# Kernel optimization log

Hardware: AMD Instinct MI355X
Metric: run time of the kernel (lower is better)

The kernel has to match this reference:

```python
import jax, jax.numpy as jnp
import numpy as np

NEG = -jnp.finfo(jnp.float32).max


def setup_inputs() -> dict:
    key = jax.random.key(0)
    ks = jax.random.split(key, 5)
    B, N, C = 8, 1024, 768
    x = jax.random.normal(ks[0], (B, N, C), dtype=jnp.float32)
    qkv_w = jax.random.normal(ks[1], (3 * C, C), dtype=jnp.float32) * (C ** -0.5)
    qkv_b = jax.random.normal(ks[2], (3 * C,), dtype=jnp.float32) * 0.02
    proj_w = jax.random.normal(ks[3], (C, C), dtype=jnp.float32) * (C ** -0.5)
    proj_b = jax.random.normal(ks[4], (C,), dtype=jnp.float32) * 0.02
    return {"x": x, "qkv_w": qkv_w, "qkv_b": qkv_b, "proj_w": proj_w, "proj_b": proj_b, "k": 64}


def reference(x, qkv_w, qkv_b, proj_w, proj_b, k):
    B, N, C = x.shape
    H = 12
    d = C // H
    scale = d ** -0.5
    # qkv projection: [B,N,3C] -> [3,B,H,N,d]
    qkv = (x @ qkv_w.T + qkv_b).reshape(B, N, 3, H, d).transpose(2, 0, 3, 1, 4)
    q, kk, v = qkv[0], qkv[1], qkv[2]
    attn = jnp.einsum("bhqd,bhkd->bhqk", q, kk) * scale  # [B,H,N,N]
    if k > 0:
        top, _ = jax.lax.top_k(attn, k)
        vk = top[..., -1:]  # k-th largest per query row
        attn = jnp.where(attn < vk, NEG, attn)
    attn = jax.nn.softmax(attn, axis=-1)
    out = jnp.einsum("bhqk,bhkd->bhqd", attn, v)  # [B,H,N,d]
    out = out.transpose(0, 2, 1, 3).reshape(B, N, C)
    return out @ proj_w.T + proj_b
```

## Files before the change

### kernel.cpp

```cpp
#include <hip/hip_runtime.h>

constexpr int Bn = 8, Nn = 1024, Cn = 768, Hn = 12, Dn = 64;

typedef _Float16 f16x4 __attribute__((ext_vector_type(4)));
typedef _Float16 f16x8 __attribute__((ext_vector_type(8)));
typedef float    f32x4v __attribute__((ext_vector_type(4)));

__device__ __forceinline__ unsigned toOrd(float f) {
  unsigned u = __float_as_uint(f);
  return (u & 0x80000000u) ? ~u : (u | 0x80000000u);
}
__device__ __forceinline__ float invOrd(unsigned v) {
  unsigned b = (v & 0x80000000u) ? (v & 0x7FFFFFFFu) : ~v;
  return __uint_as_float(b);
}
__device__ __forceinline__ int lane_excl_cnt(unsigned long long m) {
  return __builtin_amdgcn_mbcnt_hi((unsigned)(m >> 32),
         __builtin_amdgcn_mbcnt_lo((unsigned)m, 0));
}

__device__ __forceinline__ float wave_sum_f32(float x) {
  int xi = __float_as_int(x);
  x += __int_as_float(__builtin_amdgcn_update_dpp(0, xi, 0x111, 0xF, 0xF, false)); xi = __float_as_int(x);
  x += __int_as_float(__builtin_amdgcn_update_dpp(0, xi, 0x112, 0xF, 0xF, false)); xi = __float_as_int(x);
  x += __int_as_float(__builtin_amdgcn_update_dpp(0, xi, 0x114, 0xF, 0xF, false)); xi = __float_as_int(x);
  x += __int_as_float(__builtin_amdgcn_update_dpp(0, xi, 0x118, 0xF, 0xF, false)); xi = __float_as_int(x);
  x += __int_as_float(__builtin_amdgcn_update_dpp(0, xi, 0x142, 0xA, 0xF, false)); xi = __float_as_int(x);
  x += __int_as_float(__builtin_amdgcn_update_dpp(0, xi, 0x143, 0xC, 0xF, false));
  return __int_as_float(__builtin_amdgcn_readlane(__float_as_int(x), 63));
}
__device__ __forceinline__ unsigned wave_max_u32(unsigned x) {
  int xi = (int)x;
  x = max(x, (unsigned)__builtin_amdgcn_update_dpp(xi, xi, 0x111, 0xF, 0xF, false)); xi = (int)x;
  x = max(x, (unsigned)__builtin_amdgcn_update_dpp(xi, xi, 0x112, 0xF, 0xF, false)); xi = (int)x;
  x = max(x, (unsigned)__builtin_amdgcn_update_dpp(xi, xi, 0x114, 0xF, 0xF, false)); xi = (int)x;
  x = max(x, (unsigned)__builtin_amdgcn_update_dpp(xi, xi, 0x118, 0xF, 0xF, false)); xi = (int)x;
  x = max(x, (unsigned)__builtin_amdgcn_update_dpp(xi, xi, 0x142, 0xA, 0xF, false)); xi = (int)x;
  x = max(x, (unsigned)__builtin_amdgcn_update_dpp(xi, xi, 0x143, 0xC, 0xF, false));
  return (unsigned)__builtin_amdgcn_readlane((int)x, 63);
}
__device__ __forceinline__ unsigned wave_min_u32(unsigned x) {
  int xi = (int)x;
  x = min(x, (unsigned)__builtin_amdgcn_update_dpp(xi, xi, 0x111, 0xF, 0xF, false)); xi = (int)x;
  x = min(x, (unsigned)__builtin_amdgcn_update_dpp(xi, xi, 0x112, 0xF, 0xF, false)); xi = (int)x;
  x = min(x, (unsigned)__builtin_amdgcn_update_dpp(xi, xi, 0x114, 0xF, 0xF, false)); xi = (int)x;
  x = min(x, (unsigned)__builtin_amdgcn_update_dpp(xi, xi, 0x118, 0xF, 0xF, false)); xi = (int)x;
  x = min(x, (unsigned)__builtin_amdgcn_update_dpp(xi, xi, 0x142, 0xA, 0xF, false)); xi = (int)x;
  x = min(x, (unsigned)__builtin_amdgcn_update_dpp(xi, xi, 0x143, 0xC, 0xF, false));
  return (unsigned)__builtin_amdgcn_readlane((int)x, 63);
}

__global__ __launch_bounds__(256) void qkv_gemm_mfma(
    const float* __restrict__ X, const float* __restrict__ W,
    const float* __restrict__ bias,
    _Float16* __restrict__ qhp, _Float16* __restrict__ qlp,
    _Float16* __restrict__ khp, _Float16* __restrict__ klp,
    float* __restrict__ vb)
{
  constexpr int LDH = 40;
  __shared__ _Float16 AhH[128*LDH];
  __shared__ _Float16 AhL[128*LDH];
  __shared__ _Float16 BhH[64*LDH];
  __shared__ _Float16 BhL[64*LDH];
  int t = threadIdx.x;
  int wv = t >> 6, lane = t & 63;
  int quad = lane >> 4, l16 = lane & 15;
  int mt = blockIdx.x & 63, nt = blockIdx.x >> 6;
  int m0 = mt*128, n0 = nt*64;
  const float* Ap = X + (size_t)m0*768;
  const float* Bp = W + (size_t)n0*768;
  f32x4v acc1[2][4] = {};
  f32x4v acc2[2][4] = {};
  for (int k0 = 0; k0 < 768; k0 += 32) {
    float4 av[4]; float4 bv[2];
#pragma unroll
    for (int i = 0; i < 4; ++i) {
      int q = t + i*256;
      av[i] = *(const float4*)(Ap + (size_t)(q>>3)*768 + k0 + (q&7)*4);
    }
#pragma unroll
    for (int i = 0; i < 2; ++i) {
      int q = t + i*256;
      bv[i] = *(const float4*)(Bp + (size_t)(q>>3)*768 + k0 + (q&7)*4);
    }
    __syncthreads();
#pragma unroll
    for (int i = 0; i < 4; ++i) {
      int q = t + i*256;
      f16x4 h, l;
      h[0]=(_Float16)av[i].x; h[1]=(_Float16)av[i].y;
      h[2]=(_Float16)av[i].z; h[3]=(_Float16)av[i].w;
      l[0]=(_Float16)((av[i].x-(float)h[0])*2048.0f);
      l[1]=(_Float16)((av[i].y-(float)h[1])*2048.0f);
      l[2]=(_Float16)((av[i].z-(float)h[2])*2048.0f);
      l[3]=(_Float16)((av[i].w-(float)h[3])*2048.0f);
      *(f16x4*)(&AhH[(q>>3)*LDH + (q&7)*4]) = h;
      *(f16x4*)(&AhL[(q>>3)*LDH + (q&7)*4]) = l;
    }
#pragma unroll
    for (int i = 0; i < 2; ++i) {
      int q = t + i*256;
      f16x4 h, l;
      h[0]=(_Float16)bv[i].x; h[1]=(_Float16)bv[i].y;
      h[2]=(_Float16)bv[i].z; h[3]=(_Float16)bv[i].w;
      l[0]=(_Float16)((bv[i].x-(float)h[0])*2048.0f);
      l[1]=(_Float16)((bv[i].y-(float)h[1])*2048.0f);
      l[2]=(_Float16)((bv[i].z-(float)h[2])*2048.0f);
      l[3]=(_Float16)((bv[i].w-(float)h[3])*2048.0f);
      *(f16x4*)(&BhH[(q>>3)*LDH + (q&7)*4]) = h;
      *(f16x4*)(&BhL[(q>>3)*LDH + (q&7)*4]) = l;
    }
    __syncthreads();
    f16x8 bfh[4], bfl[4];
#pragma unroll
    for (int ni = 0; ni < 4; ++ni) {
      bfh[ni] = *(f16x8*)(&BhH[(ni*16+l16)*LDH + quad*8]);
      bfl[ni] = *(f16x8*)(&BhL[(ni*16+l16)*LDH + quad*8]);
    }
#pragma unroll
    for (int mi = 0; mi < 2; ++mi) {
      f16x8 afh = *(f16x8*)(&AhH[(wv*32+mi*16+l16)*LDH + quad*8]);
      f16x8 afl = *(f16x8*)(&AhL[(wv*32+mi*16+l16)*LDH + quad*8]);
#pragma unroll
      for (int ni = 0; ni < 4; ++ni) {
        acc1[mi][ni] = __builtin_amdgcn_mfma_f32_16x16x32_f16(afh, bfh[ni], acc1[mi][ni], 0, 0, 0);
        acc2[mi][ni] = __builtin_amdgcn_mfma_f32_16x16x32_f16(afh, bfl[ni], acc2[mi][ni], 0, 0, 0);
        acc2[mi][ni] = __builtin_amdgcn_mfma_f32_16x16x32_f16(afl, bfh[ni], acc2[mi][ni], 0, 0, 0);
      }
    }
  }
  int which = n0 / Cn;
  int rem0 = n0 - which*Cn;
  int h0 = rem0 >> 6;
  float sc = which == 0 ? 0.125f : 1.0f;
#pragma unroll
  for (int ni = 0; ni < 4; ++ni) {
    float bsv = bias[n0 + ni*16 + l16];
    int dd = (ni*16 + l16) & 63;
#pragma unroll
    for (int mi = 0; mi < 2; ++mi)
#pragma unroll
      for (int r = 0; r < 4; ++r) {
        int gm = m0 + wv*32 + mi*16 + quad*4 + r;
        int bbi = gm >> 10, nn = gm & 1023;
        size_t idx = (((size_t)(bbi*Hn + h0))*Nn + nn)*Dn + dd;
        float val = (acc1[mi][ni][r] + acc2[mi][ni][r] * (1.0f/2048.0f) + bsv) * sc;
        if (which == 2) {
          vb[idx] = val;
        } else {
          _Float16 hh = (_Float16)val;
          _Float16 ll = (_Float16)((val - (float)hh) * 2048.0f);
          if (which == 0) { qhp[idx] = hh; qlp[idx] = ll; }
          else            { khp[idx] = hh; klp[idx] = ll; }
        }
      }
  }
}

template <typename Epi>
__device__ __forceinline__ void mfma_gemm_body(
    const float* __restrict__ Xp, const float* __restrict__ Wp, Epi epi)
{
  constexpr int LDH = 40;
  __shared__ _Float16 Ah[128*LDH];
  __shared__ _Float16 Bh[64*LDH];
  int t = threadIdx.x;
  int wv = t >> 6, lane = t & 63;
  int quad = lane >> 4, l16 = lane & 15;
  int mt = blockIdx.x & 63, nt = blockIdx.x >> 6;
  int m0 = mt*128, n0 = nt*64;
  f32x4v acc[2][4] = {};
  for (int k0 = 0; k0 < 768; k0 += 32) {
    float4 av[4]; float4 bv[2];
#pragma unroll
    for (int i = 0; i < 4; ++i) {
      int q = t + i*256;
      av[i] = *(const float4*)(Xp + (size_t)(m0+(q>>3))*768 + k0 + (q&7)*4);
    }
#pragma unroll
    for (int i = 0; i < 2; ++i) {
      int q = t + i*256;
      bv[i] = *(const float4*)(Wp + (size_t)(n0+(q>>3))*768 + k0 + (q&7)*4);
    }
    __syncthreads();
#pragma unroll
    for (int i = 0; i < 4; ++i) {
      int q = t + i*256;
      f16x4 h; h[0]=(_Float16)av[i].x; h[1]=(_Float16)av[i].y;
               h[2]=(_Float16)av[i].z; h[3]=(_Float16)av[i].w;
      *(f16x4*)(&Ah[(q>>3)*LDH + (q&7)*4]) = h;
    }
#pragma unroll
    for (int i = 0; i < 2; ++i) {
      int q = t + i*256;
      f16x4 h; h[0]=(_Float16)bv[i].x; h[1]=(_Float16)bv[i].y;
               h[2]=(_Float16)bv[i].z; h[3]=(_Float16)bv[i].w;
      *(f16x4*)(&Bh[(q>>3)*LDH + (q&7)*4]) = h;
    }
    __syncthreads();
    f16x8 bf[4], af;
#pragma unroll
    for (int ni = 0; ni < 4; ++ni)
      bf[ni] = *(f16x8*)(&Bh[(ni*16+l16)*LDH + quad*8]);
#pragma unroll
    for (int mi = 0; mi < 2; ++mi) {
      af = *(f16x8*)(&Ah[(wv*32+mi*16+l16)*LDH + quad*8]);
#pragma unroll
      for (int ni = 0; ni < 4; ++ni)
        acc[mi][ni] = __builtin_amdgcn_mfma_f32_16x16x32_f16(af, bf[ni], acc[mi][ni], 0, 0, 0);
    }
  }
#pragma unroll
  for (int mi = 0; mi < 2; ++mi)
#pragma unroll
    for (int ni = 0; ni < 4; ++ni)
#pragma unroll
      for (int r = 0; r < 4; ++r) {
        int gm = m0 + wv*32 + mi*16 + quad*4 + r;
        int gn = n0 + ni*16 + l16;
        epi(gm, gn, acc[mi][ni][r]);
      }
}

__global__ __launch_bounds__(256) void proj_mfma(
    const float* __restrict__ Xp, const float* __restrict__ Wp,
    const float* __restrict__ bias, float* __restrict__ Out)
{
  mfma_gemm_body(Xp, Wp, [=](int gm, int gn, float val) {
    Out[(size_t)gm*768 + gn] = val + bias[gn];
  });
}

__global__ __launch_bounds__(512, 4) void attn_kernel(
    const _Float16* __restrict__ qh, const _Float16* __restrict__ ql,
    const _Float16* __restrict__ kh, const _Float16* __restrict__ kl,
    const float* __restrict__ vB, const int* __restrict__ kptr,
    float* __restrict__ out)
{
  constexpr int G = 16, CAP = 128, CAPP = CAP + 4, LD = 1028;
  __shared__ float Ws[G][LD];

  int t = threadIdx.x;
  int bh = blockIdx.x >> 6;
  int qg = blockIdx.x & 63;
  int qbase = qg * G;
  int w = t >> 6, lane = t & 63;
  int quad = lane >> 4, l16 = lane & 15;

  const _Float16* QH = qh + (size_t)bh * Nn * Dn;
  const _Float16* QL = ql + (size_t)bh * Nn * Dn;
  const _Float16* KH = kh + (size_t)bh * Nn * Dn;
  const _Float16* KL = kl + (size_t)bh * Nn * Dn;
  const float*   Vbh = vB + (size_t)bh * Nn * Dn;

  f16x8 aqh[2], aql[2];
  {
    size_t qoff = (size_t)(qbase + l16) * Dn + quad * 8;
#pragma unroll
    for (int c = 0; c < 2; ++c) {
      aqh[c] = *(const f16x8*)(QH + qoff + c*32);
      aql[c] = *(const f16x8*)(QL + qoff + c*32);
    }
  }
  f16x8 bhf[2][2], blf[2][2];
  {
    size_t koff = (size_t)(w*128 + l16) * Dn + quad*8;
#pragma unroll
    for (int c = 0; c < 2; ++c) {
      bhf[0][c] = *(const f16x8*)(KH + koff + c*32);
      blf[0][c] = *(const f16x8*)(KL + koff + c*32);
    }
  }
#pragma unroll
  for (int tt = 0; tt < 8; ++tt) {
    if (tt < 7) {
      size_t koff = (size_t)(w*128 + (tt+1)*16 + l16) * Dn + quad*8;
#pragma unroll
      for (int c = 0; c < 2; ++c) {
        bhf[(tt+1)&1][c] = *(const f16x8*)(KH + koff + c*32);
        blf[(tt+1)&1][c] = *(const f16x8*)(KL + koff + c*32);
      }
    }
    int cb = tt & 1;
    f32x4v a1 = {}, a2 = {};
    a1 = __builtin_amdgcn_mfma_f32_16x16x32_f16(aqh[0], bhf[cb][0], a1, 0,0,0);
    a1 = __builtin_amdgcn_mfma_f32_16x16x32_f16(aqh[1], bhf[cb][1], a1, 0,0,0);
    a2 = __builtin_amdgcn_mfma_f32_16x16x32_f16(aqh[0], blf[cb][0], a2, 0,0,0);
    a2 = __builtin_amdgcn_mfma_f32_16x16x32_f16(aqh[1], blf[cb][1], a2, 0,0,0);
    a2 = __builtin_amdgcn_mfma_f32_16x16x32_f16(aql[0], bhf[cb][0], a2, 0,0,0);
    a2 = __builtin_amdgcn_mfma_f32_16x16x32_f16(aql[1], bhf[cb][1], a2, 0,0,0);
    int col = w*128 + tt*16 + l16;
#pragma unroll
    for (int r2 = 0; r2 < 4; ++r2)
      Ws[quad*4 + r2][col] = a1[r2] + a2[r2] * (1.0f/2048.0f);
  }
  __syncthreads();

  int kval = *kptr;
  bool doSel = (kval > 0 && kval < Nn);

  int r0 = w*2, r1 = r0 + 1;
  unsigned u0[16], u1[16];
#pragma unroll
  for (int i = 0; i < 16; ++i) u0[i] = toOrd(Ws[r0][lane + 64*i]);
#pragma unroll
  for (int i = 0; i < 16; ++i) u1[i] = toOrd(Ws[r1][lane + 64*i]);

  unsigned mu0 = u0[0], mu1 = u1[0];
#pragma unroll
  for (int i = 1; i < 16; ++i) { mu0 = max(mu0, u0[i]); mu1 = max(mu1, u1[i]); }
  float m0 = invOrd(wave_max_u32(mu0));
  float m1 = invOrd(wave_max_u32(mu1));

  unsigned thr0 = 0u, thr1 = 0u;
  if (doSel) {
    unsigned res0 = 0u, res1 = 0u;
    bool done0 = false, done1 = false;
    for (int bit = 31; bit >= 0; --bit) {
      if (!done0) {
        unsigned cand = res0 | (1u << bit);
        int ct = 0;
#pragma unroll
        for (int i = 0; i < 16; ++i)
          ct += __popcll(__ballot(u0[i] >= cand));
        if (ct == kval) {
          unsigned mn = 0xFFFFFFFFu;
#pragma unroll
          for (int i = 0; i < 16; ++i)
            if (u0[i] >= cand && u0[i] < mn) mn = u0[i];
          res0 = wave_min_u32(mn);
          done0 = true;
        } else if (ct > kval) res0 = cand;
      }
      if (!done1) {
        unsigned cand = res1 | (1u << bit);
        int ct = 0;
#pragma unroll
        for (int i = 0; i < 16; ++i)
          ct += __popcll(__ballot(u1[i] >= cand));
        if (ct == kval) {
          unsigned mn = 0xFFFFFFFFu;
#pragma unroll
          for (int i = 0; i < 16; ++i)
            if (u1[i] >= cand && u1[i] < mn) mn = u1[i];
          res1 = wave_min_u32(mn);
          done1 = true;
        } else if (ct > kval) res1 = cand;
      }
      if (done0 && done1) break;
    }
    thr0 = res0; thr1 = res1;
  }

  float2* Pair0 = (float2*)&Ws[r0][LD - 2*CAPP];
  float2* Pair1 = (float2*)&Ws[r1][LD - 2*CAPP];
  float Zl0 = 0.f, Zl1 = 0.f;
  int cnt0 = 0, cnt1 = 0;
#pragma unroll
  for (int i = 0; i < 16; ++i) {
    bool k0 = (u0[i] >= thr0);
    unsigned long long mk0 = __ballot(k0);
    if (k0) {
      float wgt = __expf(invOrd(u0[i]) - m0);
      Zl0 += wgt;
      int pos = cnt0 + lane_excl_cnt(mk0);
      if (pos < CAP) {
        float2 pr; pr.x = wgt; pr.y = __int_as_float(lane + 64*i);
        Pair0[pos] = pr;
      }
    }
    cnt0 += __popcll(mk0);
    bool k1 = (u1[i] >= thr1);
    unsigned long long mk1 = __ballot(k1);
    if (k1) {
      float wgt = __expf(invOrd(u1[i]) - m1);
      Zl1 += wgt;
      int pos = cnt1 + lane_excl_cnt(mk1);
      if (pos < CAP) {
        float2 pr; pr.x = wgt; pr.y = __int_as_float(lane + 64*i);
        Pair1[pos] = pr;
      }
    }
    cnt1 += __popcll(mk1);
  }
  float Z0 = wave_sum_f32(Zl0);
  float Z1 = wave_sum_f32(Zl1);

  if (lane < 4) {
    float2 z; z.x = 0.f; z.y = __int_as_float(0);
    if (cnt0 <= CAP) Pair0[cnt0 + lane] = z;
    if (cnt1 <= CAP) Pair1[cnt1 + lane] = z;
  }

  float acc0 = 0.f, acc1 = 0.f;
  bool fast0 = (cnt0 <= CAP), fast1 = (cnt1 <= CAP);
  if (fast0 && fast1) {
    int nc = min(cnt0, cnt1);
    int i = 0;
    for (; i < nc; i += 4) {
      float2 p00 = Pair0[i],   p01 = Pair0[i+1];
      float2 p02 = Pair0[i+2], p03 = Pair0[i+3];
      float2 p10 = Pair1[i],   p11 = Pair1[i+1];
      float2 p12 = Pair1[i+2], p13 = Pair1[i+3];
      float v00 = Vbh[(size_t)__float_as_int(p00.y)*Dn + lane];
      float v01 = Vbh[(size_t)__float_as_int(p01.y)*Dn + lane];
      float v02 = Vbh[(size_t)__float_as_int(p02.y)*Dn + lane];
      float v03 = Vbh[(size_t)__float_as_int(p03.y)*Dn + lane];
      float v10 = Vbh[(size_t)__float_as_int(p10.y)*Dn + lane];
      float v11 = Vbh[(size_t)__float_as_int(p11.y)*Dn + lane];
      float v12 = Vbh[(size_t)__float_as_int(p12.y)*Dn + lane];
      float v13 = Vbh[(size_t)__float_as_int(p13.y)*Dn + lane];
      acc0 = fmaf(p00.x, v00, acc0); acc0 = fmaf(p01.x, v01, acc0);
      acc0 = fmaf(p02.x, v02, acc0); acc0 = fmaf(p03.x, v03, acc0);
      acc1 = fmaf(p10.x, v10, acc1); acc1 = fmaf(p11.x, v11, acc1);
      acc1 = fmaf(p12.x, v12, acc1); acc1 = fmaf(p13.x, v13, acc1);
    }
    for (; i < cnt0; i += 4) {
      float2 p0 = Pair0[i],   p1 = Pair0[i+1];
      float2 p2 = Pair0[i+2], p3 = Pair0[i+3];
      float v0 = Vbh[(size_t)__float_as_int(p0.y)*Dn + lane];
      float v1 = Vbh[(size_t)__float_as_int(p1.y)*Dn + lane];
      float v2 = Vbh[(size_t)__float_as_int(p2.y)*Dn + lane];
      float v3 = Vbh[(size_t)__float_as_int(p3.y)*Dn + lane];
      acc0 = fmaf(p0.x, v0, acc0); acc0 = fmaf(p1.x, v1, acc0);
      acc0 = fmaf(p2.x, v2, acc0); acc0 = fmaf(p3.x, v3, acc0);
    }
    for (; i < cnt1; i += 4) {
      float2 p0 = Pair1[i],   p1 = Pair1[i+1];
      float2 p2 = Pair1[i+2], p3 = Pair1[i+3];
      float v0 = Vbh[(size_t)__float_as_int(p0.y)*Dn + lane];
      float v1 = Vbh[(size_t)__float_as_int(p1.y)*Dn + lane];
      float v2 = Vbh[(size_t)__float_as_int(p2.y)*Dn + lane];
      float v3 = Vbh[(size_t)__float_as_int(p3.y)*Dn + lane];
      acc1 = fmaf(p0.x, v0, acc1); acc1 = fmaf(p1.x, v1, acc1);
      acc1 = fmaf(p2.x, v2, acc1); acc1 = fmaf(p3.x, v3, acc1);
    }
  } else {
    if (fast0) {
      for (int i = 0; i < cnt0; i += 4) {
        float2 p0 = Pair0[i],   p1 = Pair0[i+1];
        float2 p2 = Pair0[i+2], p3 = Pair0[i+3];
        float v0 = Vbh[(size_t)__float_as_int(p0.y)*Dn + lane];
        float v1 = Vbh[(size_t)__float_as_int(p1.y)*Dn + lane];
        float v2 = Vbh[(size_t)__float_as_int(p2.y)*Dn + lane];
        float v3 = Vbh[(size_t)__float_as_int(p3.y)*Dn + lane];
        acc0 = fmaf(p0.x, v0, acc0); acc0 = fmaf(p1.x, v1, acc0);
        acc0 = fmaf(p2.x, v2, acc0); acc0 = fmaf(p3.x, v3, acc0);
      }
    } else {
#pragma unroll
      for (int i = 0; i < 16; ++i)
        Ws[r0][lane + 64*i] = (u0[i] >= thr0) ? __expf(invOrd(u0[i]) - m0) : 0.f;
      for (int j = 0; j < 1024; ++j) {
        float wgt = Ws[r0][j];
        if (wgt != 0.f) acc0 = fmaf(wgt, Vbh[(size_t)j*Dn + lane], acc0);
      }
    }
    if (fast1) {
      for (int i = 0; i < cnt1; i += 4) {
        float2 p0 = Pair1[i],   p1 = Pair1[i+1];
        float2 p2 = Pair1[i+2], p3 = Pair1[i+3];
        float v0 = Vbh[(size_t)__float_as_int(p0.y)*Dn + lane];
        float v1 = Vbh[(size_t)__float_as_int(p1.y)*Dn + lane];
        float v2 = Vbh[(size_t)__float_as_int(p2.y)*Dn + lane];
        float v3 = Vbh[(size_t)__float_as_int(p3.y)*Dn + lane];
        acc1 = fmaf(p0.x, v0, acc1); acc1 = fmaf(p1.x, v1, acc1);
        acc1 = fmaf(p2.x, v2, acc1); acc1 = fmaf(p3.x, v3, acc1);
      }
    } else {
#pragma unroll
      for (int i = 0; i < 16; ++i)
        Ws[r1][lane + 64*i] = (u1[i] >= thr1) ? __expf(invOrd(u1[i]) - m1) : 0.f;
      for (int j = 0; j < 1024; ++j) {
        float wgt = Ws[r1][j];
        if (wgt != 0.f) acc1 = fmaf(wgt, Vbh[(size_t)j*Dn + lane], acc1);
      }
    }
  }

  int b = bh / Hn, h = bh - b*Hn;
  out[((size_t)(b*Nn + qbase + r0))*Cn + h*Dn + lane] = acc0 * (1.0f / Z0);
  out[((size_t)(b*Nn + qbase + r1))*Cn + h*Dn + lane] = acc1 * (1.0f / Z1);
}

extern "C" void kernel_launch(void* const* d_in, const int* in_sizes, int n_in,
                              void* d_out, int out_size, void* d_ws, size_t ws_size,
                              hipStream_t stream) {
  const float* x      = (const float*)d_in[0];
  const float* qkv_w  = (const float*)d_in[1];
  const float* qkv_b  = (const float*)d_in[2];
  const float* proj_w = (const float*)d_in[3];
  const float* proj_b = (const float*)d_in[4];
  const int*   kptr   = (const int*)d_in[5];

  const size_t sz = (size_t)Bn * Hn * Nn * Dn;
  _Float16* qh = (_Float16*)d_ws;
  _Float16* ql = qh + sz;
  _Float16* kh = ql + sz;
  _Float16* kl = kh + sz;
  float* vbuf  = (float*)(kl + sz);
  float* att   = vbuf + sz;
  float* outp  = (float*)d_out;

  qkv_gemm_mfma<<<dim3(36*64), 256, 0, stream>>>(x, qkv_w, qkv_b,
                                                 qh, ql, kh, kl, vbuf);
  attn_kernel<<<dim3(Bn*Hn*(Nn/16)), 512, 0, stream>>>(qh, ql, kh, kl,
                                                       vbuf, kptr, att);
  proj_mfma<<<dim3(12*64), 256, 0, stream>>>(att, proj_w, proj_b, outp);
}
```

Before: 595.4 us.

## Shrink attention LDS footprint with double-buffered score tiles to raise occupancy

The 16x1028 float score buffer in shared memory (~64KB) is replaced by a small double-buffered 16x132 staging tile plus a separate pair buffer. Each of the 8 QK iterations writes a 128-column slice, syncs, and each wave pulls its rows' values straight into registers. The dense fallback path now broadcasts weights with wave shuffles instead of staging them in shared memory. The launch-bounds target goes from 4 to 8 blocks per CU to exploit the smaller LDS use, at the cost of a barrier per iteration and tighter register pressure.

```diff
diff --git a/kernel.cpp b/kernel.cpp
--- a/kernel.cpp
+++ b/kernel.cpp
@@ -231,14 +231,15 @@
   });
 }
 
-__global__ __launch_bounds__(512, 4) void attn_kernel(
+__global__ __launch_bounds__(512, 8) void attn_kernel(
     const _Float16* __restrict__ qh, const _Float16* __restrict__ ql,
     const _Float16* __restrict__ kh, const _Float16* __restrict__ kl,
     const float* __restrict__ vB, const int* __restrict__ kptr,
     float* __restrict__ out)
 {
-  constexpr int G = 16, CAP = 128, CAPP = CAP + 4, LD = 1028;
-  __shared__ float Ws[G][LD];
+  constexpr int G = 16, CAP = 128, CAPP = CAP + 4, LDB = 132;
+  __shared__ float  Bx[2][G][LDB];
+  __shared__ float2 PairS[G][CAPP];
 
   int t = threadIdx.x;
   int bh = blockIdx.x >> 6;
@@ -253,6 +254,9 @@
   const _Float16* KL = kl + (size_t)bh * Nn * Dn;
   const float*   Vbh = vB + (size_t)bh * Nn * Dn;
 
+  int r0 = w*2, r1 = r0 + 1;
+  unsigned u0[16], u1[16];
+
   f16x8 aqh[2], aql[2];
   {
     size_t qoff = (size_t)(qbase + l16) * Dn + quad * 8;
@@ -264,7 +268,7 @@
   }
   f16x8 bhf[2][2], blf[2][2];
   {
-    size_t koff = (size_t)(w*128 + l16) * Dn + quad*8;
+    size_t koff = (size_t)(16*w + l16) * Dn + quad*8;
 #pragma unroll
     for (int c = 0; c < 2; ++c) {
       bhf[0][c] = *(const f16x8*)(KH + koff + c*32);
@@ -272,16 +276,16 @@
     }
   }
 #pragma unroll
-  for (int tt = 0; tt < 8; ++tt) {
-    if (tt < 7) {
-      size_t koff = (size_t)(w*128 + (tt+1)*16 + l16) * Dn + quad*8;
+  for (int j = 0; j < 8; ++j) {
+    if (j < 7) {
+      size_t koff = (size_t)(16*w + 128*(j+1) + l16) * Dn + quad*8;
 #pragma unroll
       for (int c = 0; c < 2; ++c) {
-        bhf[(tt+1)&1][c] = *(const f16x8*)(KH + koff + c*32);
-        blf[(tt+1)&1][c] = *(const f16x8*)(KL + koff + c*32);
-      }
-    }
-    int cb = tt & 1;
+        bhf[(j+1)&1][c] = *(const f16x8*)(KH + koff + c*32);
+        blf[(j+1)&1][c] = *(const f16x8*)(KL + koff + c*32);
+      }
+    }
+    int cb = j & 1;
     f32x4v a1 = {}, a2 = {};
     a1 = __builtin_amdgcn_mfma_f32_16x16x32_f16(aqh[0], bhf[cb][0], a1, 0,0,0);
     a1 = __builtin_amdgcn_mfma_f32_16x16x32_f16(aqh[1], bhf[cb][1], a1, 0,0,0);
@@ -289,22 +293,18 @@
     a2 = __builtin_amdgcn_mfma_f32_16x16x32_f16(aqh[1], blf[cb][1], a2, 0,0,0);
     a2 = __builtin_amdgcn_mfma_f32_16x16x32_f16(aql[0], bhf[cb][0], a2, 0,0,0);
     a2 = __builtin_amdgcn_mfma_f32_16x16x32_f16(aql[1], bhf[cb][1], a2, 0,0,0);
-    int col = w*128 + tt*16 + l16;
 #pragma unroll
     for (int r2 = 0; r2 < 4; ++r2)
-      Ws[quad*4 + r2][col] = a1[r2] + a2[r2] * (1.0f/2048.0f);
-  }
-  __syncthreads();
+      Bx[cb][quad*4 + r2][w*16 + l16] = a1[r2] + a2[r2] * (1.0f/2048.0f);
+    __syncthreads();
+    u0[2*j]   = toOrd(Bx[cb][r0][lane]);
+    u0[2*j+1] = toOrd(Bx[cb][r0][lane + 64]);
+    u1[2*j]   = toOrd(Bx[cb][r1][lane]);
+    u1[2*j+1] = toOrd(Bx[cb][r1][lane + 64]);
+  }
 
   int kval = *kptr;
   bool doSel = (kval > 0 && kval < Nn);
-
-  int r0 = w*2, r1 = r0 + 1;
-  unsigned u0[16], u1[16];
-#pragma unroll
-  for (int i = 0; i < 16; ++i) u0[i] = toOrd(Ws[r0][lane + 64*i]);
-#pragma unroll
-  for (int i = 0; i < 16; ++i) u1[i] = toOrd(Ws[r1][lane + 64*i]);
 
   unsigned mu0 = u0[0], mu1 = u1[0];
 #pragma unroll
@@ -352,8 +352,8 @@
     thr0 = res0; thr1 = res1;
   }
 
-  float2* Pair0 = (float2*)&Ws[r0][LD - 2*CAPP];
-  float2* Pair1 = (float2*)&Ws[r1][LD - 2*CAPP];
+  float2* Pair0 = &PairS[r0][0];
+  float2* Pair1 = &PairS[r1][0];
   float Zl0 = 0.f, Zl1 = 0.f;
   int cnt0 = 0, cnt1 = 0;
 #pragma unroll
@@ -449,11 +449,13 @@
       }
     } else {
 #pragma unroll
-      for (int i = 0; i < 16; ++i)
-        Ws[r0][lane + 64*i] = (u0[i] >= thr0) ? __expf(invOrd(u0[i]) - m0) : 0.f;
-      for (int j = 0; j < 1024; ++j) {
-        float wgt = Ws[r0][j];
-        if (wgt != 0.f) acc0 = fmaf(wgt, Vbh[(size_t)j*Dn + lane], acc0);
+      for (int i = 0; i < 16; ++i) {
+        float wbase = (u0[i] >= thr0) ? __expf(invOrd(u0[i]) - m0) : 0.f;
+        for (int src = 0; src < 64; ++src) {
+          float wgt = __shfl(wbase, src);
+          if (wgt != 0.f)
+            acc0 = fmaf(wgt, Vbh[(size_t)(src + 64*i)*Dn + lane], acc0);
+        }
       }
     }
     if (fast1) {
@@ -469,11 +471,13 @@
       }
     } else {
 #pragma unroll
-      for (int i = 0; i < 16; ++i)
-        Ws[r1][lane + 64*i] = (u1[i] >= thr1) ? __expf(invOrd(u1[i]) - m1) : 0.f;
-      for (int j = 0; j < 1024; ++j) {
-        float wgt = Ws[r1][j];
-        if (wgt != 0.f) acc1 = fmaf(wgt, Vbh[(size_t)j*Dn + lane], acc1);
+      for (int i = 0; i < 16; ++i) {
+        float wbase = (u1[i] >= thr1) ? __expf(invOrd(u1[i]) - m1) : 0.f;
+        for (int src = 0; src < 64; ++src) {
+          float wgt = __shfl(wbase, src);
+          if (wgt != 0.f)
+            acc1 = fmaf(wgt, Vbh[(size_t)(src + 64*i)*Dn + lane], acc1);
+        }
       }
     }
   }
```

After: 529.3 us. 1.12x faster.
